# Kernel optimization log

Measured on AMD Instinct MI355X. Metric: run time of the kernel, lower is better.

The kernel has to match this reference:

```python
import jax, jax.numpy as jnp
import numpy as np

N_NODES = 100000
N_EDGES = 1600000
D_FEAT = 128
CONV1_OUT = 64
CONV2_OUT = 32


def setup_inputs() -> dict:
    key = jax.random.key(0)
    k1, k2, k3, k4, k5, k6 = jax.random.split(key, 6)
    x = jax.random.normal(k1, (N_NODES, D_FEAT), dtype=jnp.float32)
    edge_row = jax.random.randint(k2, (N_EDGES,), 0, N_NODES, dtype=jnp.int32)
    edge_col = jax.random.randint(k3, (N_EDGES,), 0, N_NODES, dtype=jnp.int32)
    # normalized adjacency values (D^-1/2 A D^-1/2 entries are small positives)
    edge_val = jax.random.uniform(k4, (N_EDGES,), dtype=jnp.float32) / 16.0
    w1 = jax.random.normal(k5, (D_FEAT, CONV1_OUT), dtype=jnp.float32) / np.sqrt(D_FEAT)
    w2 = jax.random.normal(k6, (CONV1_OUT, CONV2_OUT), dtype=jnp.float32) / np.sqrt(CONV1_OUT)
    return {"x": x, "edge_row": edge_row, "edge_col": edge_col,
            "edge_val": edge_val, "w1": w1, "w2": w2}


def _spmm(edge_row, edge_col, edge_val, h):
    # out[i] = sum_{e: row[e]==i} val[e] * h[col[e]]  (sparse A @ h)
    gathered = edge_val[:, None] * h[edge_col]          # [E, F]
    return jax.ops.segment_sum(gathered, edge_row, num_segments=N_NODES)


def reference(x, edge_row, edge_col, edge_val, w1, w2):
    # Layer 1 (shared weights, relu); dropout inactive at inference.
    h = jnp.relu if False else None  # placeholder to keep linter quiet
    h1 = jax.nn.relu(_spmm(edge_row, edge_col, edge_val, x @ w1))   # [N, 64]
    # Layer 2 (per-cluster, identity activation)
    out = _spmm(edge_row, edge_col, edge_val, h1 @ w2)              # [N, 32]
    return out
```

## Files before the change

### kernel.cpp

```cpp
#include <hip/hip_runtime.h>

#define D_FEAT 128
#define C1 64
#define C2 32
#define BROWS 256
#define LOG_BROWS 8
#define BCAP  4608
#define NBMAX 512
#define GSTRIDE 16
#define CHUNK 8192
#define PT 512
#define EPT (CHUNK / PT)
#define WPAD 136
#define HPAD 72
#define VSCALE (32767.0f * 16.0f)
#define VDEQ (1.0f / VSCALE)

using bf16x8 = __attribute__((ext_vector_type(8))) __bf16;
using f32x4  = __attribute__((ext_vector_type(4))) float;

__device__ __forceinline__ unsigned short f2bf(float f) {
    unsigned u = __float_as_uint(f);
    u += 0x7fff + ((u >> 16) & 1);
    return (unsigned short)(u >> 16);
}
__device__ __forceinline__ float bflo(unsigned u) {
    return __uint_as_float(u << 16);
}
__device__ __forceinline__ float bfhi(unsigned u) {
    return __uint_as_float(u & 0xffff0000u);
}

__global__ __launch_bounds__(256) void zero_gcur(int* __restrict__ g, int count) {
    int i = blockIdx.x * 256 + threadIdx.x;
    if (i < count) g[i] = 0;
}

union PartGemmSM {
    struct { int hist[NBMAX]; int base[NBMAX]; int cnt[NBMAX]; } p;
    struct { unsigned short wsb[C1][WPAD]; unsigned short xs[128][WPAD]; } g;
};

__global__ __launch_bounds__(PT) void part_gemm1(const int* __restrict__ row,
                                                 const int* __restrict__ col,
                                                 const float* __restrict__ val,
                                                 int* __restrict__ gcur,
                                                 int2* __restrict__ bucket,
                                                 const float* __restrict__ A,
                                                 const float* __restrict__ W,
                                                 unsigned short* __restrict__ C,
                                                 int E, int nb, int n, int pblocks) {
    __shared__ PartGemmSM sm;
    const int t = threadIdx.x;

    if ((int)blockIdx.x < pblocks) {
        const long long e0 = (long long)blockIdx.x * CHUNK;
        for (int i = t; i < nb; i += PT) {
            sm.p.hist[i] = 0;
            sm.p.cnt[i] = 0;
        }
        __syncthreads();

        #pragma unroll
        for (int k = 0; k < EPT; k++) {
            long long i = e0 + (long long)k * PT + t;
            if (i < E) atomicAdd(&sm.p.hist[row[i] >> LOG_BROWS], 1);
        }
        __syncthreads();

        for (int i = t; i < nb; i += PT)
            if (sm.p.hist[i] > 0)
                sm.p.base[i] = atomicAdd(&gcur[i * GSTRIDE], sm.p.hist[i]);
        __syncthreads();

        #pragma unroll
        for (int k = 0; k < EPT; k++) {
            long long i = e0 + (long long)k * PT + t;
            if (i < E) {
                int rr = row[i];
                int b = rr >> LOG_BROWS;
                int off = sm.p.base[b] + atomicAdd(&sm.p.cnt[b], 1);
                if (off < BCAP)
                    bucket[(size_t)b * BCAP + off] =
                        make_int2(((rr & (BROWS - 1)) << 17) | col[i],
                                  __float_as_int(val[i]));
            }
        }
    } else {
        const int lane = t & 63;
        const int w    = t >> 6;
        const int row0 = ((int)blockIdx.x - pblocks) * 128;

        #pragma unroll
        for (int it = 0; it < 4; ++it) {
            const int nc = t & 63;
            const int k0 = ((t >> 6) + 8 * it) * 4;
            ushort4 o;
            o.x = f2bf(W[(k0 + 0) * C1 + nc]);
            o.y = f2bf(W[(k0 + 1) * C1 + nc]);
            o.z = f2bf(W[(k0 + 2) * C1 + nc]);
            o.w = f2bf(W[(k0 + 3) * C1 + nc]);
            *(ushort4*)&sm.g.wsb[nc][k0] = o;
        }

        #pragma unroll
        for (int it = 0; it < 8; ++it) {
            const int qi = it * PT + t;
            const int r  = qi >> 5;
            const int kq = (qi & 31) * 4;
            const int gr = row0 + r;
            float4 v = make_float4(0.f, 0.f, 0.f, 0.f);
            if (gr < n)
                v = *(const float4*)(A + (size_t)gr * D_FEAT + kq);
            ushort4 o;
            o.x = f2bf(v.x); o.y = f2bf(v.y); o.z = f2bf(v.z); o.w = f2bf(v.w);
            *(ushort4*)&sm.g.xs[r][kq] = o;
        }
        __syncthreads();

        f32x4 acc[4];
        #pragma unroll
        for (int ct = 0; ct < 4; ++ct)
            acc[ct] = (f32x4){0.f, 0.f, 0.f, 0.f};

        const int mr = w * 16 + (lane & 15);
        const int kq = (lane >> 4) * 8;
        #pragma unroll
        for (int ks = 0; ks < 4; ++ks) {
            bf16x8 av = *(const bf16x8*)&sm.g.xs[mr][ks * 32 + kq];
            #pragma unroll
            for (int ct = 0; ct < 4; ++ct) {
                bf16x8 bv = *(const bf16x8*)&sm.g.wsb[ct * 16 + (lane & 15)][ks * 32 + kq];
                acc[ct] = __builtin_amdgcn_mfma_f32_16x16x32_bf16(av, bv, acc[ct], 0, 0, 0);
            }
        }

        const int rowbase = row0 + w * 16 + (lane >> 4) * 4;
        #pragma unroll
        for (int j = 0; j < 4; ++j) {
            const int gr = rowbase + j;
            if (gr < n) {
                #pragma unroll
                for (int ct = 0; ct < 4; ++ct)
                    C[(size_t)gr * C1 + ct * 16 + (lane & 15)] = f2bf(acc[ct][j]);
            }
        }
    }
}

__global__ __launch_bounds__(512) void bucket_scan(const int* __restrict__ gcur,
                                                   int* __restrict__ bstart, int nb) {
    __shared__ int s[512];
    const int t = threadIdx.x;
    int v = (t < nb) ? gcur[t * GSTRIDE] : 0;
    s[t] = v;
    __syncthreads();
    for (int off = 1; off < 512; off <<= 1) {
        int x = (t >= off) ? s[t - off] : 0;
        __syncthreads();
        s[t] += x;
        __syncthreads();
    }
    if (t < nb) bstart[t] = s[t] - v;
}

__global__ __launch_bounds__(256) void bucket_place(const int* __restrict__ gcur,
                                                    const int* __restrict__ bstart,
                                                    const int2* __restrict__ bucket,
                                                    int* __restrict__ ptr,
                                                    unsigned* __restrict__ csr, int n) {
    __shared__ int rhist[BROWS];
    __shared__ int rcur[BROWS];
    __shared__ int sscan[BROWS];
    __shared__ unsigned lbuf[BCAP];
    const int b = blockIdx.x;
    const int t = threadIdx.x;
    const int cnt = min(gcur[b * GSTRIDE], BCAP);
    const int gbase = bstart[b];
    const int2* bb = bucket + (size_t)b * BCAP;

    rhist[t] = 0;
    __syncthreads();

    for (int j = t; j < cnt; j += 256)
        atomicAdd(&rhist[bb[j].x >> 17], 1);
    __syncthreads();

    const int v = rhist[t];
    sscan[t] = v;
    __syncthreads();
    for (int off = 1; off < 256; off <<= 1) {
        int x = (t >= off) ? sscan[t - off] : 0;
        __syncthreads();
        sscan[t] += x;
        __syncthreads();
    }
    const int excl = sscan[t] - v;
    rcur[t] = excl;
    const int r0 = b * BROWS + t;
    if (r0 < n) ptr[r0] = gbase + excl;
    __syncthreads();

    for (int j = t; j < cnt; j += 256) {
        int2 w = bb[j];
        int lr = w.x >> 17;
        int pos = atomicAdd(&rcur[lr], 1);
        float fv = __int_as_float(w.y);
        unsigned vq = (unsigned)__float2int_rn(fv * VSCALE);
        vq = min(vq, 32767u);
        lbuf[pos] = ((unsigned)(w.x & 0x1FFFF) << 15) | vq;
    }
    __syncthreads();

    for (int j = t; j < cnt; j += 256)
        csr[(size_t)gbase + j] = lbuf[j];
}

__global__ __launch_bounds__(256) void spmm64_fused(const int* __restrict__ ptr,
                                                    const unsigned* __restrict__ csr,
                                                    const uint4* __restrict__ Hb,
                                                    const float* __restrict__ W2,
                                                    unsigned short* __restrict__ Zb,
                                                    int n, int E) {
    __shared__ unsigned short hlds[32][HPAD];
    __shared__ unsigned short w2t[C2][HPAD];

    const int t    = threadIdx.x;
    const int lane = t & 63;
    const int w    = t >> 6;
    const int g    = lane >> 3;
    const int lp   = lane & 7;
    const int rloc = w * 8 + g;
    const int row  = blockIdx.x * 32 + rloc;

    {
        const int nc = t & 31;
        const int k0 = (t >> 5) * 8;
        #pragma unroll
        for (int i = 0; i < 8; ++i)
            w2t[nc][k0 + i] = f2bf(W2[(k0 + i) * C2 + nc]);
    }

    int start = 0, end = 0;
    if (row < n) {
        start = ptr[row];
        end   = (row + 1 < n) ? ptr[row + 1] : E;
    }

    float A0 = 0.f, A1 = 0.f, A2 = 0.f, A3 = 0.f;
    float A4 = 0.f, A5 = 0.f, A6 = 0.f, A7 = 0.f;
    int e = start;
    for (; e + 7 < end; e += 8) {
        unsigned c[8];
        uint4 G[8];
        #pragma unroll
        for (int q = 0; q < 8; q++) c[q] = csr[e + q];
        #pragma unroll
        for (int q = 0; q < 8; q++) G[q] = Hb[(size_t)(c[q] >> 15) * 8 + lp];
        #pragma unroll
        for (int q = 0; q < 8; q++) {
            float v = (float)(c[q] & 0x7FFF) * VDEQ;
            A0 += v * bflo(G[q].x); A1 += v * bfhi(G[q].x);
            A2 += v * bflo(G[q].y); A3 += v * bfhi(G[q].y);
            A4 += v * bflo(G[q].z); A5 += v * bfhi(G[q].z);
            A6 += v * bflo(G[q].w); A7 += v * bfhi(G[q].w);
        }
    }
    if (e + 3 < end) {
        unsigned c[4];
        uint4 G[4];
        #pragma unroll
        for (int q = 0; q < 4; q++) c[q] = csr[e + q];
        #pragma unroll
        for (int q = 0; q < 4; q++) G[q] = Hb[(size_t)(c[q] >> 15) * 8 + lp];
        #pragma unroll
        for (int q = 0; q < 4; q++) {
            float v = (float)(c[q] & 0x7FFF) * VDEQ;
            A0 += v * bflo(G[q].x); A1 += v * bfhi(G[q].x);
            A2 += v * bflo(G[q].y); A3 += v * bfhi(G[q].y);
            A4 += v * bflo(G[q].z); A5 += v * bfhi(G[q].z);
            A6 += v * bflo(G[q].w); A7 += v * bfhi(G[q].w);
        }
        e += 4;
    }
    for (; e < end; e++) {
        unsigned c = csr[e];
        uint4 gg = Hb[(size_t)(c >> 15) * 8 + lp];
        float v = (float)(c & 0x7FFF) * VDEQ;
        A0 += v * bflo(gg.x); A1 += v * bfhi(gg.x);
        A2 += v * bflo(gg.y); A3 += v * bfhi(gg.y);
        A4 += v * bflo(gg.z); A5 += v * bfhi(gg.z);
        A6 += v * bflo(gg.w); A7 += v * bfhi(gg.w);
    }

    {
        ushort4 o0, o1;
        o0.x = f2bf(fmaxf(A0, 0.f)); o0.y = f2bf(fmaxf(A1, 0.f));
        o0.z = f2bf(fmaxf(A2, 0.f)); o0.w = f2bf(fmaxf(A3, 0.f));
        o1.x = f2bf(fmaxf(A4, 0.f)); o1.y = f2bf(fmaxf(A5, 0.f));
        o1.z = f2bf(fmaxf(A6, 0.f)); o1.w = f2bf(fmaxf(A7, 0.f));
        *(ushort4*)&hlds[rloc][lp * 8]     = o0;
        *(ushort4*)&hlds[rloc][lp * 8 + 4] = o1;
    }
    __syncthreads();

    if (w < 2) {
        f32x4 acc[2];
        acc[0] = (f32x4){0.f, 0.f, 0.f, 0.f};
        acc[1] = (f32x4){0.f, 0.f, 0.f, 0.f};
        const int kq = (lane >> 4) * 8;
        #pragma unroll
        for (int ks = 0; ks < 2; ++ks) {
            bf16x8 av = *(const bf16x8*)&hlds[w * 16 + (lane & 15)][ks * 32 + kq];
            #pragma unroll
            for (int ct = 0; ct < 2; ++ct) {
                bf16x8 bv = *(const bf16x8*)&w2t[ct * 16 + (lane & 15)][ks * 32 + kq];
                acc[ct] = __builtin_amdgcn_mfma_f32_16x16x32_bf16(av, bv, acc[ct], 0, 0, 0);
            }
        }
        #pragma unroll
        for (int j = 0; j < 4; ++j) {
            const int grow = blockIdx.x * 32 + w * 16 + (lane >> 4) * 4 + j;
            if (grow < n) {
                #pragma unroll
                for (int ct = 0; ct < 2; ++ct)
                    Zb[(size_t)grow * C2 + ct * 16 + (lane & 15)] = f2bf(acc[ct][j]);
            }
        }
    }
}

__global__ __launch_bounds__(256) void spmm_csr32(const int* __restrict__ ptr,
                                                  const unsigned* __restrict__ csr,
                                                  const uint2* __restrict__ Zb,
                                                  float* __restrict__ OUT, int n, int E) {
    const int tid  = blockIdx.x * 256 + threadIdx.x;
    const int gwid = tid >> 6;
    const int lane = threadIdx.x & 63;
    const int g    = lane >> 3;
    const int lp   = lane & 7;
    const int row  = gwid * 8 + g;

    int start = 0, end = 0;
    if (row < n) {
        start = ptr[row];
        end   = (row + 1 < n) ? ptr[row + 1] : E;
    }

    float a0 = 0.f, a1 = 0.f, a2 = 0.f, a3 = 0.f;
    int e = start;
    for (; e + 7 < end; e += 8) {
        unsigned c[8];
        uint2 G[8];
        #pragma unroll
        for (int q = 0; q < 8; q++) c[q] = csr[e + q];
        #pragma unroll
        for (int q = 0; q < 8; q++) G[q] = Zb[(size_t)(c[q] >> 15) * 8 + lp];
        #pragma unroll
        for (int q = 0; q < 8; q++) {
            float v = (float)(c[q] & 0x7FFF) * VDEQ;
            a0 += v * bflo(G[q].x); a1 += v * bfhi(G[q].x);
            a2 += v * bflo(G[q].y); a3 += v * bfhi(G[q].y);
        }
    }
    if (e + 3 < end) {
        unsigned c[4];
        uint2 G[4];
        #pragma unroll
        for (int q = 0; q < 4; q++) c[q] = csr[e + q];
        #pragma unroll
        for (int q = 0; q < 4; q++) G[q] = Zb[(size_t)(c[q] >> 15) * 8 + lp];
        #pragma unroll
        for (int q = 0; q < 4; q++) {
            float v = (float)(c[q] & 0x7FFF) * VDEQ;
            a0 += v * bflo(G[q].x); a1 += v * bfhi(G[q].x);
            a2 += v * bflo(G[q].y); a3 += v * bfhi(G[q].y);
        }
        e += 4;
    }
    for (; e < end; e++) {
        unsigned c = csr[e];
        uint2 gg = Zb[(size_t)(c >> 15) * 8 + lp];
        float v = (float)(c & 0x7FFF) * VDEQ;
        a0 += v * bflo(gg.x); a1 += v * bfhi(gg.x);
        a2 += v * bflo(gg.y); a3 += v * bfhi(gg.y);
    }
    if (row < n)
        *(float4*)(OUT + (size_t)row * C2 + 4 * lp) = make_float4(a0, a1, a2, a3);
}

extern "C" void kernel_launch(void* const* d_in, const int* in_sizes, int n_in,
                              void* d_out, int out_size, void* d_ws, size_t ws_size,
                              hipStream_t stream) {
    const float* x    = (const float*)d_in[0];
    const int*   erow = (const int*)d_in[1];
    const int*   ecol = (const int*)d_in[2];
    const float* eval = (const float*)d_in[3];
    const float* w1   = (const float*)d_in[4];
    const float* w2   = (const float*)d_in[5];
    float* out = (float*)d_out;

    const int n = in_sizes[0] / D_FEAT;
    const int E = in_sizes[1];

    const int nb = (n + BROWS - 1) / BROWS;
    const int pblocks = (E + CHUNK - 1) / CHUNK;
    const int gblocks = (n + 127) / 128;

    unsigned short* y1b = (unsigned short*)d_ws;
    int2*  bucket = (int2*)(y1b + (size_t)n * C1);
    unsigned* csr = (unsigned*)(bucket + (size_t)nb * BCAP);
    int*   ptr    = (int*)(csr + E);
    int*   gcur   = ptr + n + 64;
    int*   bstart = gcur + NBMAX * GSTRIDE;
    unsigned short* zb = (unsigned short*)(bstart + NBMAX);

    {
        int count = nb * GSTRIDE;
        zero_gcur<<<(count + 255) / 256, 256, 0, stream>>>(gcur, count);
    }
    part_gemm1<<<pblocks + gblocks, PT, 0, stream>>>(erow, ecol, eval, gcur, bucket,
                                                     x, w1, y1b, E, nb, n, pblocks);
    bucket_scan<<<1, 512, 0, stream>>>(gcur, bstart, nb);
    bucket_place<<<nb, 256, 0, stream>>>(gcur, bstart, bucket, ptr, csr, n);

    spmm64_fused<<<(n + 31) / 32, 256, 0, stream>>>(ptr, csr, (const uint4*)y1b,
                                                    w2, zb, n, E);

    {
        int rows_per_block = 32;
        int blocks = (n + rows_per_block - 1) / rows_per_block;
        spmm_csr32<<<blocks, 256, 0, stream>>>(ptr, csr, (const uint2*)zb,
                                               out, n, E);
    }
}
```

Before: 108.9 us.

## Stage bucketed edges in shared memory for coalesced global scatter

The partition phase now sorts each chunk's edges locally by bucket, using an LDS prefix scan over the histogram and a shared staging buffer. It then writes them to the global bucket array in contiguous runs, so stores land in adjacent addresses instead of scattering randomly. Row indices are kept in registers to avoid reloading them, and CHUNK is halved so the staging buffer fits in LDS, which doubles the number of partition blocks and global atomics. The scan adds extra barriers, and the larger shared footprint may lower occupancy.

```diff
diff --git a/kernel.cpp b/kernel.cpp
--- a/kernel.cpp
+++ b/kernel.cpp
@@ -8,7 +8,7 @@
 #define BCAP  4608
 #define NBMAX 512
 #define GSTRIDE 16
-#define CHUNK 8192
+#define CHUNK 4096
 #define PT 512
 #define EPT (CHUNK / PT)
 #define WPAD 136
@@ -37,7 +37,14 @@
 }
 
 union PartGemmSM {
-    struct { int hist[NBMAX]; int base[NBMAX]; int cnt[NBMAX]; } p;
+    struct {
+        int hist[NBMAX];
+        int lstart[NBMAX];
+        int gbase[NBMAX];
+        int cnt[NBMAX];
+        int2 lbuf[CHUNK];
+        unsigned short bid[CHUNK];
+    } p;
     struct { unsigned short wsb[C1][WPAD]; unsigned short xs[128][WPAD]; } g;
 };
 
@@ -55,36 +62,63 @@
 
     if ((int)blockIdx.x < pblocks) {
         const long long e0 = (long long)blockIdx.x * CHUNK;
+        const int total = (int)min((long long)CHUNK, (long long)E - e0);
+
         for (int i = t; i < nb; i += PT) {
             sm.p.hist[i] = 0;
             sm.p.cnt[i] = 0;
         }
         __syncthreads();
 
+        int r[EPT];
         #pragma unroll
         for (int k = 0; k < EPT; k++) {
             long long i = e0 + (long long)k * PT + t;
-            if (i < E) atomicAdd(&sm.p.hist[row[i] >> LOG_BROWS], 1);
+            r[k] = (i < E) ? row[i] : -1;
+            if (r[k] >= 0) atomicAdd(&sm.p.hist[r[k] >> LOG_BROWS], 1);
         }
         __syncthreads();
 
         for (int i = t; i < nb; i += PT)
             if (sm.p.hist[i] > 0)
-                sm.p.base[i] = atomicAdd(&gcur[i * GSTRIDE], sm.p.hist[i]);
-        __syncthreads();
+                sm.p.gbase[i] = atomicAdd(&gcur[i * GSTRIDE], sm.p.hist[i]);
+
+        {
+            int v = (t < nb) ? sm.p.hist[t] : 0;
+            sm.p.lstart[t < NBMAX ? t : 0] = 0;
+            sm.p.lstart[t] = v;
+            __syncthreads();
+            int run = v;
+            for (int off = 1; off < PT; off <<= 1) {
+                int x = (t >= off) ? sm.p.lstart[t - off] : 0;
+                __syncthreads();
+                sm.p.lstart[t] += x;
+                __syncthreads();
+            }
+            int incl = sm.p.lstart[t];
+            __syncthreads();
+            sm.p.lstart[t] = incl - run;
+            __syncthreads();
+        }
 
         #pragma unroll
         for (int k = 0; k < EPT; k++) {
             long long i = e0 + (long long)k * PT + t;
-            if (i < E) {
-                int rr = row[i];
-                int b = rr >> LOG_BROWS;
-                int off = sm.p.base[b] + atomicAdd(&sm.p.cnt[b], 1);
-                if (off < BCAP)
-                    bucket[(size_t)b * BCAP + off] =
-                        make_int2(((rr & (BROWS - 1)) << 17) | col[i],
-                                  __float_as_int(val[i]));
-            }
+            if (r[k] >= 0) {
+                int b = r[k] >> LOG_BROWS;
+                int p = sm.p.lstart[b] + atomicAdd(&sm.p.cnt[b], 1);
+                sm.p.lbuf[p] = make_int2(((r[k] & (BROWS - 1)) << 17) | col[i],
+                                         __float_as_int(val[i]));
+                sm.p.bid[p] = (unsigned short)b;
+            }
+        }
+        __syncthreads();
+
+        for (int j = t; j < total; j += PT) {
+            int b = sm.p.bid[j];
+            int off = sm.p.gbase[b] + (j - sm.p.lstart[b]);
+            if (off < BCAP)
+                bucket[(size_t)b * BCAP + off] = sm.p.lbuf[j];
         }
     } else {
         const int lane = t & 63;
```

Measured after the change: 108.4 us. About the same (-0.4%).

## Pre-convert W1 to bf16 in prep kernel and drop LDS staging in GEMM

Applied to the files above, without the earlier changes.

The zero-init kernel now also writes a transposed bf16 copy of W1 to workspace, so the GEMM blocks no longer convert W1 per block. The GEMM path loads X rows and W1 fragments directly from global memory into MFMA operands, which removes the shared-memory staging and the barrier and shrinks the LDS union to just the histogram arrays. The partition path keeps row indices in registers instead of reloading them. Direct global loads of X give strided, non-coalesced access per lane and rely on cache for reuse of W1, but the smaller LDS footprint may allow higher occupancy.

```diff
diff --git a/kernel.cpp b/kernel.cpp
--- a/kernel.cpp
+++ b/kernel.cpp
@@ -11,7 +11,6 @@
 #define CHUNK 8192
 #define PT 512
 #define EPT (CHUNK / PT)
-#define WPAD 136
 #define HPAD 72
 #define VSCALE (32767.0f * 16.0f)
 #define VDEQ (1.0f / VSCALE)
@@ -31,15 +30,17 @@
     return __uint_as_float(u & 0xffff0000u);
 }
 
-__global__ __launch_bounds__(256) void zero_gcur(int* __restrict__ g, int count) {
+__global__ __launch_bounds__(256) void zero_prep(int* __restrict__ g, int count,
+                                                 const float* __restrict__ W,
+                                                 unsigned short* __restrict__ w1t) {
     int i = blockIdx.x * 256 + threadIdx.x;
     if (i < count) g[i] = 0;
-}
-
-union PartGemmSM {
-    struct { int hist[NBMAX]; int base[NBMAX]; int cnt[NBMAX]; } p;
-    struct { unsigned short wsb[C1][WPAD]; unsigned short xs[128][WPAD]; } g;
-};
+    if (i < C1 * D_FEAT) {
+        int nc = i >> 7;
+        int k  = i & 127;
+        w1t[i] = f2bf(W[k * C1 + nc]);
+    }
+}
 
 __global__ __launch_bounds__(PT) void part_gemm1(const int* __restrict__ row,
                                                  const int* __restrict__ col,
@@ -47,42 +48,45 @@
                                                  int* __restrict__ gcur,
                                                  int2* __restrict__ bucket,
                                                  const float* __restrict__ A,
-                                                 const float* __restrict__ W,
+                                                 const unsigned short* __restrict__ w1t,
                                                  unsigned short* __restrict__ C,
                                                  int E, int nb, int n, int pblocks) {
-    __shared__ PartGemmSM sm;
+    __shared__ int hist[NBMAX];
+    __shared__ int base[NBMAX];
+    __shared__ int cnt[NBMAX];
     const int t = threadIdx.x;
 
     if ((int)blockIdx.x < pblocks) {
         const long long e0 = (long long)blockIdx.x * CHUNK;
         for (int i = t; i < nb; i += PT) {
-            sm.p.hist[i] = 0;
-            sm.p.cnt[i] = 0;
-        }
-        __syncthreads();
-
+            hist[i] = 0;
+            cnt[i] = 0;
+        }
+        __syncthreads();
+
+        int r[EPT];
         #pragma unroll
         for (int k = 0; k < EPT; k++) {
             long long i = e0 + (long long)k * PT + t;
-            if (i < E) atomicAdd(&sm.p.hist[row[i] >> LOG_BROWS], 1);
+            r[k] = (i < E) ? row[i] : -1;
+            if (r[k] >= 0) atomicAdd(&hist[r[k] >> LOG_BROWS], 1);
         }
         __syncthreads();
 
         for (int i = t; i < nb; i += PT)
-            if (sm.p.hist[i] > 0)
-                sm.p.base[i] = atomicAdd(&gcur[i * GSTRIDE], sm.p.hist[i]);
+            if (hist[i] > 0)
+                base[i] = atomicAdd(&gcur[i * GSTRIDE], hist[i]);
         __syncthreads();
 
         #pragma unroll
         for (int k = 0; k < EPT; k++) {
             long long i = e0 + (long long)k * PT + t;
-            if (i < E) {
-                int rr = row[i];
-                int b = rr >> LOG_BROWS;
-                int off = sm.p.base[b] + atomicAdd(&sm.p.cnt[b], 1);
+            if (r[k] >= 0) {
+                int b = r[k] >> LOG_BROWS;
+                int off = base[b] + atomicAdd(&cnt[b], 1);
                 if (off < BCAP)
                     bucket[(size_t)b * BCAP + off] =
-                        make_int2(((rr & (BROWS - 1)) << 17) | col[i],
+                        make_int2(((r[k] & (BROWS - 1)) << 17) | col[i],
                                   __float_as_int(val[i]));
             }
         }
@@ -91,58 +95,44 @@
         const int w    = t >> 6;
         const int row0 = ((int)blockIdx.x - pblocks) * 128;
 
-        #pragma unroll
-        for (int it = 0; it < 4; ++it) {
-            const int nc = t & 63;
-            const int k0 = ((t >> 6) + 8 * it) * 4;
-            ushort4 o;
-            o.x = f2bf(W[(k0 + 0) * C1 + nc]);
-            o.y = f2bf(W[(k0 + 1) * C1 + nc]);
-            o.z = f2bf(W[(k0 + 2) * C1 + nc]);
-            o.w = f2bf(W[(k0 + 3) * C1 + nc]);
-            *(ushort4*)&sm.g.wsb[nc][k0] = o;
-        }
-
-        #pragma unroll
-        for (int it = 0; it < 8; ++it) {
-            const int qi = it * PT + t;
-            const int r  = qi >> 5;
-            const int kq = (qi & 31) * 4;
-            const int gr = row0 + r;
-            float4 v = make_float4(0.f, 0.f, 0.f, 0.f);
-            if (gr < n)
-                v = *(const float4*)(A + (size_t)gr * D_FEAT + kq);
-            ushort4 o;
-            o.x = f2bf(v.x); o.y = f2bf(v.y); o.z = f2bf(v.z); o.w = f2bf(v.w);
-            *(ushort4*)&sm.g.xs[r][kq] = o;
-        }
-        __syncthreads();
+        const int gr = row0 + w * 16 + (lane & 15);
+        const int kq = (lane >> 4) * 8;
 
         f32x4 acc[4];
         #pragma unroll
         for (int ct = 0; ct < 4; ++ct)
             acc[ct] = (f32x4){0.f, 0.f, 0.f, 0.f};
 
-        const int mr = w * 16 + (lane & 15);
-        const int kq = (lane >> 4) * 8;
         #pragma unroll
         for (int ks = 0; ks < 4; ++ks) {
-            bf16x8 av = *(const bf16x8*)&sm.g.xs[mr][ks * 32 + kq];
+            union { unsigned short s[8]; bf16x8 v; } av;
+            if (gr < n) {
+                const float* xp = A + (size_t)gr * D_FEAT + ks * 32 + kq;
+                float4 a0 = *(const float4*)(xp);
+                float4 a1 = *(const float4*)(xp + 4);
+                av.s[0] = f2bf(a0.x); av.s[1] = f2bf(a0.y);
+                av.s[2] = f2bf(a0.z); av.s[3] = f2bf(a0.w);
+                av.s[4] = f2bf(a1.x); av.s[5] = f2bf(a1.y);
+                av.s[6] = f2bf(a1.z); av.s[7] = f2bf(a1.w);
+            } else {
+                av.v = (bf16x8)(__bf16)0.0f;
+            }
             #pragma unroll
             for (int ct = 0; ct < 4; ++ct) {
-                bf16x8 bv = *(const bf16x8*)&sm.g.wsb[ct * 16 + (lane & 15)][ks * 32 + kq];
-                acc[ct] = __builtin_amdgcn_mfma_f32_16x16x32_bf16(av, bv, acc[ct], 0, 0, 0);
+                bf16x8 bv = *(const bf16x8*)&w1t[(ct * 16 + (lane & 15)) * D_FEAT
+                                                 + ks * 32 + kq];
+                acc[ct] = __builtin_amdgcn_mfma_f32_16x16x32_bf16(av.v, bv, acc[ct], 0, 0, 0);
             }
         }
 
         const int rowbase = row0 + w * 16 + (lane >> 4) * 4;
         #pragma unroll
         for (int j = 0; j < 4; ++j) {
-            const int gr = rowbase + j;
-            if (gr < n) {
+            const int go = rowbase + j;
+            if (go < n) {
                 #pragma unroll
                 for (int ct = 0; ct < 4; ++ct)
-                    C[(size_t)gr * C1 + ct * 16 + (lane & 15)] = f2bf(acc[ct][j]);
+                    C[(size_t)go * C1 + ct * 16 + (lane & 15)] = f2bf(acc[ct][j]);
             }
         }
     }
@@ -413,14 +403,17 @@
     int*   ptr    = (int*)(csr + E);
     int*   gcur   = ptr + n + 64;
     int*   bstart = gcur + NBMAX * GSTRIDE;
-    unsigned short* zb = (unsigned short*)(bstart + NBMAX);
+    unsigned short* w1t = (unsigned short*)(bstart + NBMAX);
+    unsigned short* zb  = w1t + C1 * D_FEAT;
 
     {
         int count = nb * GSTRIDE;
-        zero_gcur<<<(count + 255) / 256, 256, 0, stream>>>(gcur, count);
-    }
+        int total = max(count, C1 * D_FEAT);
+        zero_prep<<<(total + 255) / 256, 256, 0, stream>>>(gcur, count, w1, w1t);
+    }
+
     part_gemm1<<<pblocks + gblocks, PT, 0, stream>>>(erow, ecol, eval, gcur, bucket,
-                                                     x, w1, y1b, E, nb, n, pblocks);
+                                                     x, w1t, y1b, E, nb, n, pblocks);
     bucket_scan<<<1, 512, 0, stream>>>(gcur, bstart, nb);
     bucket_place<<<nb, 256, 0, stream>>>(gcur, bstart, bucket, ptr, csr, n);
 
```

After: 113.5 us. +4.3%, slower.

## Halve GEMM tile rows, split columns across waves, cache row indices in registers

Applied to the files above, without the earlier changes.

The GEMM branch of the fused partition/GEMM kernel now handles 64 rows per block instead of 128, with 8 waves split into 4 row quads by 2 column pairs, so twice as many GEMM blocks run with less LDS each. The W staging loop is remapped so consecutive threads read consecutive k for a given output column. The partition branch keeps each edge's row index in registers between the histogram and scatter passes instead of loading it from global memory twice. The cost is more blocks that each stage the full W matrix, and more registers per thread in the partition path.

```diff
diff --git a/kernel.cpp b/kernel.cpp
--- a/kernel.cpp
+++ b/kernel.cpp
@@ -38,7 +38,7 @@
 
 union PartGemmSM {
     struct { int hist[NBMAX]; int base[NBMAX]; int cnt[NBMAX]; } p;
-    struct { unsigned short wsb[C1][WPAD]; unsigned short xs[128][WPAD]; } g;
+    struct { unsigned short wsb[C1][WPAD]; unsigned short xs[64][WPAD]; } g;
 };
 
 __global__ __launch_bounds__(PT) void part_gemm1(const int* __restrict__ row,
@@ -61,10 +61,12 @@
         }
         __syncthreads();
 
+        int r[EPT];
         #pragma unroll
         for (int k = 0; k < EPT; k++) {
             long long i = e0 + (long long)k * PT + t;
-            if (i < E) atomicAdd(&sm.p.hist[row[i] >> LOG_BROWS], 1);
+            r[k] = (i < E) ? row[i] : -1;
+            if (r[k] >= 0) atomicAdd(&sm.p.hist[r[k] >> LOG_BROWS], 1);
         }
         __syncthreads();
 
@@ -76,25 +78,25 @@
         #pragma unroll
         for (int k = 0; k < EPT; k++) {
             long long i = e0 + (long long)k * PT + t;
-            if (i < E) {
-                int rr = row[i];
-                int b = rr >> LOG_BROWS;
+            if (r[k] >= 0) {
+                int b = r[k] >> LOG_BROWS;
                 int off = sm.p.base[b] + atomicAdd(&sm.p.cnt[b], 1);
                 if (off < BCAP)
                     bucket[(size_t)b * BCAP + off] =
-                        make_int2(((rr & (BROWS - 1)) << 17) | col[i],
+                        make_int2(((r[k] & (BROWS - 1)) << 17) | col[i],
                                   __float_as_int(val[i]));
             }
         }
     } else {
         const int lane = t & 63;
         const int w    = t >> 6;
-        const int row0 = ((int)blockIdx.x - pblocks) * 128;
+        const int row0 = ((int)blockIdx.x - pblocks) * 64;
 
         #pragma unroll
         for (int it = 0; it < 4; ++it) {
-            const int nc = t & 63;
-            const int k0 = ((t >> 6) + 8 * it) * 4;
+            const int qi = it * PT + t;
+            const int nc = qi >> 5;
+            const int k0 = (qi & 31) * 4;
             ushort4 o;
             o.x = f2bf(W[(k0 + 0) * C1 + nc]);
             o.y = f2bf(W[(k0 + 1) * C1 + nc]);
@@ -104,7 +106,7 @@
         }
 
         #pragma unroll
-        for (int it = 0; it < 8; ++it) {
+        for (int it = 0; it < 4; ++it) {
             const int qi = it * PT + t;
             const int r  = qi >> 5;
             const int kq = (qi & 31) * 4;
@@ -118,31 +120,35 @@
         }
         __syncthreads();
 
-        f32x4 acc[4];
-        #pragma unroll
-        for (int ct = 0; ct < 4; ++ct)
-            acc[ct] = (f32x4){0.f, 0.f, 0.f, 0.f};
-
-        const int mr = w * 16 + (lane & 15);
+        const int rquad = w & 3;
+        const int cpair = w >> 2;
+
+        f32x4 acc[2];
+        acc[0] = (f32x4){0.f, 0.f, 0.f, 0.f};
+        acc[1] = (f32x4){0.f, 0.f, 0.f, 0.f};
+
+        const int mr = rquad * 16 + (lane & 15);
         const int kq = (lane >> 4) * 8;
         #pragma unroll
         for (int ks = 0; ks < 4; ++ks) {
             bf16x8 av = *(const bf16x8*)&sm.g.xs[mr][ks * 32 + kq];
             #pragma unroll
-            for (int ct = 0; ct < 4; ++ct) {
+            for (int cc = 0; cc < 2; ++cc) {
+                const int ct = cpair * 2 + cc;
                 bf16x8 bv = *(const bf16x8*)&sm.g.wsb[ct * 16 + (lane & 15)][ks * 32 + kq];
-                acc[ct] = __builtin_amdgcn_mfma_f32_16x16x32_bf16(av, bv, acc[ct], 0, 0, 0);
+                acc[cc] = __builtin_amdgcn_mfma_f32_16x16x32_bf16(av, bv, acc[cc], 0, 0, 0);
             }
         }
 
-        const int rowbase = row0 + w * 16 + (lane >> 4) * 4;
+        const int rowbase = row0 + rquad * 16 + (lane >> 4) * 4;
         #pragma unroll
         for (int j = 0; j < 4; ++j) {
             const int gr = rowbase + j;
             if (gr < n) {
                 #pragma unroll
-                for (int ct = 0; ct < 4; ++ct)
-                    C[(size_t)gr * C1 + ct * 16 + (lane & 15)] = f2bf(acc[ct][j]);
+                for (int cc = 0; cc < 2; ++cc)
+                    C[(size_t)gr * C1 + (cpair * 2 + cc) * 16 + (lane & 15)]
+                        = f2bf(acc[cc][j]);
             }
         }
     }
@@ -405,7 +411,7 @@
 
     const int nb = (n + BROWS - 1) / BROWS;
     const int pblocks = (E + CHUNK - 1) / CHUNK;
-    const int gblocks = (n + 127) / 128;
+    const int gblocks = (n + 63) / 64;
 
     unsigned short* y1b = (unsigned short*)d_ws;
     int2*  bucket = (int2*)(y1b + (size_t)n * C1);
```

Measured after the change: 122.8 us. 1.13x slower.
